# Optimization experiments

Hardware: AMD Instinct MI355X
Metric: run time of the kernel (lower is better)

## Reference

```python
import jax, jax.numpy as jnp
import numpy as np

BINS = 10


def setup_inputs() -> dict:
    key = jax.random.key(0)
    k1, k2 = jax.random.split(key)
    N = 16777216
    x = jax.random.normal(k1, (N, 1), dtype=jnp.float32)
    target = jax.random.randint(k2, (N,), 0, 2, dtype=jnp.int32)
    return {"x": x, "target": target}


def reference(x, target):
    # GHMC_Loss forward (binary, num_classes=1), first call (_last_bin_count is None).
    N = x.shape[0]
    logits = x[:, 0]                                   # [N]
    t = target.astype(x.dtype)                         # [N]

    # gradient norm g = |sigmoid(x) - t|  (detached in original)
    g = jnp.abs(jax.nn.sigmoid(logits) - t)            # [N]
    bin_idx = jnp.clip(
        jnp.floor(g * (BINS - 0.0001)).astype(jnp.int32), 0, BINS - 1
    )                                                  # [N]

    # single-pass histogram via scatter-add
    bin_count = jnp.zeros((BINS,), x.dtype).at[bin_idx].add(1.0)
    nonempty = (bin_count > 0).sum().astype(x.dtype)
    gd = jnp.maximum(bin_count * nonempty, 1e-6)
    beta = jnp.asarray(N, x.dtype) / gd                # [BINS]
    weights = beta[bin_idx]                            # [N] gather

    # stable BCE with logits: logaddexp(0, x) - x*t
    ce = jnp.logaddexp(jnp.zeros_like(logits), logits) - logits * t
    return jnp.mean(ce * weights)
```

## Files before the change

kernel.cpp:

```cpp
#include <hip/hip_runtime.h>

#define BINS 10
#define TPB 256
#define VEC_ITERS 16

__global__ __launch_bounds__(64) void ghmc_zero(float* ws) {
    if (threadIdx.x < 2 * BINS) ws[threadIdx.x] = 0.0f;
}

__device__ __forceinline__ void ghmc_accum(float z, int t, float2* acc, int tid) {
    float tf = (float)t;
    float az = fabsf(z);
    float e  = __expf(-az);
    float q  = 1.0f + e;
    float r  = __builtin_amdgcn_rcpf(q);
    float s  = (z >= 0.0f) ? r : e * r;
    float g  = fabsf(s - tf);
    int bin  = (int)(g * 9.9999f);
    bin = bin < (BINS - 1) ? bin : (BINS - 1);
    float ce = fmaxf(z, 0.0f) - z * tf + __logf(q);
    int i = bin * TPB + tid;
    float2 v = acc[i];
    v.x += ce;
    v.y += 1.0f;
    acc[i] = v;
}

__global__ __launch_bounds__(TPB) void ghmc_main(const float* __restrict__ x,
                                                 const int* __restrict__ tgt,
                                                 float* __restrict__ gsum,
                                                 float* __restrict__ gcnt,
                                                 int nvec, int ntotal) {
    __shared__ float2 acc[BINS * TPB];
    const int tid = threadIdx.x;
    #pragma unroll
    for (int b = 0; b < BINS; ++b) acc[b * TPB + tid] = make_float2(0.0f, 0.0f);

    const float4* __restrict__ x4 = (const float4*)x;
    const int4*  __restrict__ t4 = (const int4*)tgt;
    const int base = blockIdx.x * (TPB * VEC_ITERS) + tid;

    #pragma unroll 4
    for (int j = 0; j < VEC_ITERS; ++j) {
        int gi = base + j * TPB;
        if (gi < nvec) {
            float4 xv = x4[gi];
            int4   tv = t4[gi];
            ghmc_accum(xv.x, tv.x, acc, tid);
            ghmc_accum(xv.y, tv.y, acc, tid);
            ghmc_accum(xv.z, tv.z, acc, tid);
            ghmc_accum(xv.w, tv.w, acc, tid);
        }
    }
    if (blockIdx.x == 0) {
        for (int i = nvec * 4 + tid; i < ntotal; i += TPB) {
            ghmc_accum(x[i], tgt[i], acc, tid);
        }
    }

    __syncthreads();
    for (int sft = TPB / 2; sft > 0; sft >>= 1) {
        if (tid < sft) {
            #pragma unroll
            for (int b = 0; b < BINS; ++b) {
                float2 a = acc[b * TPB + tid];
                float2 o = acc[b * TPB + tid + sft];
                a.x += o.x;
                a.y += o.y;
                acc[b * TPB + tid] = a;
            }
        }
        __syncthreads();
    }
    if (tid < BINS) {
        atomicAdd(&gsum[tid], acc[tid * TPB].x);
        atomicAdd(&gcnt[tid], acc[tid * TPB].y);
    }
}

__global__ __launch_bounds__(64) void ghmc_final(const float* __restrict__ gsum,
                                                 const float* __restrict__ gcnt,
                                                 float* __restrict__ out) {
    int t = threadIdx.x;
    float cnt = (t < BINS) ? gcnt[t] : 0.0f;
    float sum = (t < BINS) ? gsum[t] : 0.0f;
    float ne  = (cnt > 0.0f) ? 1.0f : 0.0f;
    #pragma unroll
    for (int o = 32; o > 0; o >>= 1) ne += __shfl_down(ne, o);
    ne = __shfl(ne, 0);
    float term = (t < BINS) ? sum / fmaxf(cnt * ne, 1e-6f) : 0.0f;
    #pragma unroll
    for (int o = 32; o > 0; o >>= 1) term += __shfl_down(term, o);
    if (t == 0) out[0] = term;
}

extern "C" void kernel_launch(void* const* d_in, const int* in_sizes, int n_in,
                              void* d_out, int out_size, void* d_ws, size_t ws_size,
                              hipStream_t stream) {
    const float* x   = (const float*)d_in[0];
    const int*   tgt = (const int*)d_in[1];
    float* out  = (float*)d_out;
    float* gsum = (float*)d_ws;
    float* gcnt = gsum + BINS;

    int N    = in_sizes[0];
    int nvec = N / 4;
    int blocks = (nvec + TPB * VEC_ITERS - 1) / (TPB * VEC_ITERS);
    if (blocks < 1) blocks = 1;

    ghmc_zero<<<1, 64, 0, stream>>>(gsum);
    ghmc_main<<<blocks, TPB, 0, stream>>>(x, tgt, gsum, gcnt, nvec, N);
    ghmc_final<<<1, 64, 0, stream>>>(gsum, gcnt, out);
}
```

Measured before the change: 167.6 us.

## Keep per-bin accumulators in registers and use grid-stride partials

Per-thread bin accumulators move from a shared-memory array indexed by bin to 20 registers, updated with a predicated unrolled loop over all bins. The main kernel becomes a grid-stride loop over at most 2048 blocks and writes per-block partials instead of using global atomics. This removes the zero kernel and replaces the shared-memory tree reduction with wave shuffles. The trade is about ten times more ALU work per element (masked FMAs across all bins) and higher register pressure, in exchange for no LDS traffic during accumulation.

```diff
diff --git a/kernel.cpp b/kernel.cpp
--- a/kernel.cpp
+++ b/kernel.cpp
@@ -2,13 +2,9 @@
 
 #define BINS 10
 #define TPB 256
-#define VEC_ITERS 16
+#define MAX_BLOCKS 2048
 
-__global__ __launch_bounds__(64) void ghmc_zero(float* ws) {
-    if (threadIdx.x < 2 * BINS) ws[threadIdx.x] = 0.0f;
-}
-
-__device__ __forceinline__ void ghmc_accum(float z, int t, float2* acc, int tid) {
+__device__ __forceinline__ void ghmc_accum(float z, int t, float* ssum, float* scnt) {
     float tf = (float)t;
     float az = fabsf(z);
     float e  = __expf(-az);
@@ -19,79 +15,106 @@
     int bin  = (int)(g * 9.9999f);
     bin = bin < (BINS - 1) ? bin : (BINS - 1);
     float ce = fmaxf(z, 0.0f) - z * tf + __logf(q);
-    int i = bin * TPB + tid;
-    float2 v = acc[i];
-    v.x += ce;
-    v.y += 1.0f;
-    acc[i] = v;
+    #pragma unroll
+    for (int b = 0; b < BINS; ++b) {
+        float mf = (bin == b) ? 1.0f : 0.0f;
+        ssum[b] = fmaf(mf, ce, ssum[b]);
+        scnt[b] += mf;
+    }
 }
 
 __global__ __launch_bounds__(TPB) void ghmc_main(const float* __restrict__ x,
                                                  const int* __restrict__ tgt,
-                                                 float* __restrict__ gsum,
-                                                 float* __restrict__ gcnt,
+                                                 float* __restrict__ partial,
                                                  int nvec, int ntotal) {
-    __shared__ float2 acc[BINS * TPB];
-    const int tid = threadIdx.x;
+    float ssum[BINS], scnt[BINS];
     #pragma unroll
-    for (int b = 0; b < BINS; ++b) acc[b * TPB + tid] = make_float2(0.0f, 0.0f);
+    for (int b = 0; b < BINS; ++b) { ssum[b] = 0.0f; scnt[b] = 0.0f; }
 
     const float4* __restrict__ x4 = (const float4*)x;
     const int4*  __restrict__ t4 = (const int4*)tgt;
-    const int base = blockIdx.x * (TPB * VEC_ITERS) + tid;
+    const int tid = threadIdx.x;
+    const int stride = gridDim.x * TPB;
 
-    #pragma unroll 4
-    for (int j = 0; j < VEC_ITERS; ++j) {
-        int gi = base + j * TPB;
-        if (gi < nvec) {
-            float4 xv = x4[gi];
-            int4   tv = t4[gi];
-            ghmc_accum(xv.x, tv.x, acc, tid);
-            ghmc_accum(xv.y, tv.y, acc, tid);
-            ghmc_accum(xv.z, tv.z, acc, tid);
-            ghmc_accum(xv.w, tv.w, acc, tid);
+    #pragma unroll 2
+    for (int gi = blockIdx.x * TPB + tid; gi < nvec; gi += stride) {
+        float4 xv = x4[gi];
+        int4   tv = t4[gi];
+        ghmc_accum(xv.x, tv.x, ssum, scnt);
+        ghmc_accum(xv.y, tv.y, ssum, scnt);
+        ghmc_accum(xv.z, tv.z, ssum, scnt);
+        ghmc_accum(xv.w, tv.w, ssum, scnt);
+    }
+    if (blockIdx.x == 0) {
+        for (int i = nvec * 4 + tid; i < ntotal; i += TPB)
+            ghmc_accum(x[i], tgt[i], ssum, scnt);
+    }
+
+    #pragma unroll
+    for (int b = 0; b < BINS; ++b) {
+        #pragma unroll
+        for (int o = 32; o > 0; o >>= 1) {
+            ssum[b] += __shfl_down(ssum[b], o);
+            scnt[b] += __shfl_down(scnt[b], o);
         }
     }
-    if (blockIdx.x == 0) {
-        for (int i = nvec * 4 + tid; i < ntotal; i += TPB) {
-            ghmc_accum(x[i], tgt[i], acc, tid);
+    __shared__ float red[TPB / 64][2 * BINS];
+    const int wid = tid >> 6, lane = tid & 63;
+    if (lane == 0) {
+        #pragma unroll
+        for (int b = 0; b < BINS; ++b) {
+            red[wid][b]        = ssum[b];
+            red[wid][BINS + b] = scnt[b];
         }
     }
-
     __syncthreads();
-    for (int sft = TPB / 2; sft > 0; sft >>= 1) {
-        if (tid < sft) {
-            #pragma unroll
-            for (int b = 0; b < BINS; ++b) {
-                float2 a = acc[b * TPB + tid];
-                float2 o = acc[b * TPB + tid + sft];
-                a.x += o.x;
-                a.y += o.y;
-                acc[b * TPB + tid] = a;
-            }
-        }
-        __syncthreads();
-    }
-    if (tid < BINS) {
-        atomicAdd(&gsum[tid], acc[tid * TPB].x);
-        atomicAdd(&gcnt[tid], acc[tid * TPB].y);
+    if (tid < 2 * BINS) {
+        float v = 0.0f;
+        #pragma unroll
+        for (int w = 0; w < TPB / 64; ++w) v += red[w][tid];
+        partial[blockIdx.x * (2 * BINS) + tid] = v;
     }
 }
 
-__global__ __launch_bounds__(64) void ghmc_final(const float* __restrict__ gsum,
-                                                 const float* __restrict__ gcnt,
-                                                 float* __restrict__ out) {
-    int t = threadIdx.x;
-    float cnt = (t < BINS) ? gcnt[t] : 0.0f;
-    float sum = (t < BINS) ? gsum[t] : 0.0f;
-    float ne  = (cnt > 0.0f) ? 1.0f : 0.0f;
+__global__ __launch_bounds__(TPB) void ghmc_final(const float* __restrict__ partial,
+                                                  float* __restrict__ out, int nblocks) {
+    float acc[2 * BINS];
     #pragma unroll
-    for (int o = 32; o > 0; o >>= 1) ne += __shfl_down(ne, o);
-    ne = __shfl(ne, 0);
-    float term = (t < BINS) ? sum / fmaxf(cnt * ne, 1e-6f) : 0.0f;
+    for (int k = 0; k < 2 * BINS; ++k) acc[k] = 0.0f;
+    for (int row = threadIdx.x; row < nblocks; row += TPB) {
+        const float* p = partial + row * (2 * BINS);
+        #pragma unroll
+        for (int k = 0; k < 2 * BINS; ++k) acc[k] += p[k];
+    }
     #pragma unroll
-    for (int o = 32; o > 0; o >>= 1) term += __shfl_down(term, o);
-    if (t == 0) out[0] = term;
+    for (int k = 0; k < 2 * BINS; ++k) {
+        #pragma unroll
+        for (int o = 32; o > 0; o >>= 1) acc[k] += __shfl_down(acc[k], o);
+    }
+    __shared__ float red[TPB / 64][2 * BINS];
+    const int wid = threadIdx.x >> 6, lane = threadIdx.x & 63;
+    if (lane == 0) {
+        #pragma unroll
+        for (int k = 0; k < 2 * BINS; ++k) red[wid][k] = acc[k];
+    }
+    __syncthreads();
+    if (threadIdx.x == 0) {
+        float ne = 0.0f;
+        float sum[BINS], cnt[BINS];
+        #pragma unroll
+        for (int b = 0; b < BINS; ++b) {
+            float s = 0.0f, c = 0.0f;
+            #pragma unroll
+            for (int w = 0; w < TPB / 64; ++w) { s += red[w][b]; c += red[w][BINS + b]; }
+            sum[b] = s; cnt[b] = c;
+            ne += (c > 0.0f) ? 1.0f : 0.0f;
+        }
+        float res = 0.0f;
+        #pragma unroll
+        for (int b = 0; b < BINS; ++b)
+            res += sum[b] / fmaxf(cnt[b] * ne, 1e-6f);
+        out[0] = res;
+    }
 }
 
 extern "C" void kernel_launch(void* const* d_in, const int* in_sizes, int n_in,
@@ -99,16 +122,19 @@
                               hipStream_t stream) {
     const float* x   = (const float*)d_in[0];
     const int*   tgt = (const int*)d_in[1];
-    float* out  = (float*)d_out;
-    float* gsum = (float*)d_ws;
-    float* gcnt = gsum + BINS;
+    float* out     = (float*)d_out;
+    float* partial = (float*)d_ws;
 
     int N    = in_sizes[0];
     int nvec = N / 4;
-    int blocks = (nvec + TPB * VEC_ITERS - 1) / (TPB * VEC_ITERS);
+
+    int blocks = MAX_BLOCKS;
+    int maxrows = (int)(ws_size / (2 * BINS * sizeof(float)));
+    if (blocks > maxrows) blocks = maxrows;
+    int need = (nvec + TPB - 1) / TPB;
+    if (blocks > need) blocks = need;
     if (blocks < 1) blocks = 1;
 
-    ghmc_zero<<<1, 64, 0, stream>>>(gsum);
-    ghmc_main<<<blocks, TPB, 0, stream>>>(x, tgt, gsum, gcnt, nvec, N);
-    ghmc_final<<<1, 64, 0, stream>>>(gsum, gcnt, out);
+    ghmc_main<<<blocks, TPB, 0, stream>>>(x, tgt, partial, nvec, N);
+    ghmc_final<<<1, TPB, 0, stream>>>(partial, out, blocks);
 }
```

New measurement: 155.8 us. 7.0% less time.
